# Kernel optimization log

Measured on AMD Instinct MI355X. Metric: run time of the kernel, lower is better.

## Reference

```python
import jax, jax.numpy as jnp
import numpy as np

B, DIMX, DIMY, DIMH = 256, 128, 128, 128
SMOOTH, CONVEX = 2.0, 1.0
MAX_IT, TOL = 500, 1e-3
sp = jax.nn.softplus


def setup_inputs() -> dict:
    key = jax.random.key(0)
    ks = jax.random.split(key, 32)
    def p(k, *shape):
        # xavier-ish small init for weights/biases
        return (jax.random.normal(k, shape, dtype=jnp.float32) * 0.05)
    return {
        'x': jax.random.normal(ks[0], (B, DIMX), dtype=jnp.float32),
        'y': jax.random.normal(ks[1], (B, DIMY), dtype=jnp.float32),
        # first block (Wuus[0], Wyus[0], Wys[0], Wus[0])
        'wuu0_w': p(ks[2], DIMH, DIMX), 'wuu0_b': p(ks[3], DIMH),
        'wyu0_w': p(ks[4], DIMY, DIMX), 'wyu0_b': p(ks[5], DIMY),
        'wy0': p(ks[6], DIMH, DIMY),
        'wu0_w': p(ks[7], DIMH, DIMX), 'wu0_b': p(ks[8], DIMH),
        # middle block (Wuus[1], Wzus[0], Wzs[0], Wyus[1], Wys[1], Wus[1])
        'wuu1_w': p(ks[9], DIMH, DIMH), 'wuu1_b': p(ks[10], DIMH),
        'wzu1_w': p(ks[11], DIMH, DIMH), 'wzu1_b': p(ks[12], DIMH),
        'wz1': p(ks[13], DIMH, DIMH),
        'wyu1_w': p(ks[14], DIMY, DIMH), 'wyu1_b': p(ks[15], DIMY),
        'wy1': p(ks[16], DIMH, DIMY),
        'wu1_w': p(ks[17], DIMH, DIMH), 'wu1_b': p(ks[18], DIMH),
        # last block (Wzus[-1], Wzs[-1], Wyus[-1], Wys[-1], Wus[-1])
        'wzu2_w': p(ks[19], 1, DIMH), 'wzu2_b': p(ks[20], 1),
        'wz2': p(ks[21], 1, DIMH),
        'wyu2_w': p(ks[22], DIMY, DIMH), 'wyu2_b': p(ks[23], DIMY),
        'wy2': p(ks[24], 1, DIMY),
        'wu2_w': p(ks[25], 1, DIMH), 'wu2_b': p(ks[26], 1),
    }


def reference(x, y, wuu0_w, wuu0_b, wyu0_w, wyu0_b, wy0, wu0_w, wu0_b,
              wuu1_w, wuu1_b, wzu1_w, wzu1_b, wz1, wyu1_w, wyu1_b, wy1, wu1_w, wu1_b,
              wzu2_w, wzu2_b, wz2, wyu2_w, wyu2_b, wy2, wu2_w, wu2_b):
    # ICNN scalar output summed over batch (per-sample outputs decouple in y)
    def icnn_sum(y_):
        u0 = sp(x @ wuu0_w.T + wuu0_b)                                   # [B,H]
        z = sp((y_ * (x @ wyu0_w.T + wyu0_b)) @ wy0.T + x @ wu0_w.T + wu0_b)
        u1 = sp(u0 @ wuu1_w.T + wuu1_b)
        zu = sp(u0 @ wzu1_w.T + wzu1_b)
        z = sp((z * zu) @ jnp.clip(wz1, 0.0, 1e10).T
               + (y_ * (u0 @ wyu1_w.T + wyu1_b)) @ wy1.T
               + u0 @ wu1_w.T + wu1_b)
        zu2 = sp(u1 @ wzu2_w.T + wzu2_b)                                 # [B,1]
        z = ((z * zu2) @ jnp.clip(wz2, 0.0, 1e10).T
             + (y_ * (u1 @ wyu2_w.T + wyu2_b)) @ wy2.T
             + u1 @ wu2_w.T + wu2_b)                                     # [B,1]
        out = z + (0.5 / SMOOTH) * jnp.sum(y_ * y_, axis=1, keepdims=True)
        return jnp.sum(out)

    grad_icnn = jax.grad(icnn_sum)
    step = 2.0 * SMOOTH

    def body(carry, i):
        y1, done = carry
        g = grad_icnn(y1)
        y1_new = y1 + (step / (i + 1.0)) * (y - g)
        conv = jnp.mean(jnp.linalg.norm(y - g, axis=1)) < TOL
        y1 = jnp.where(done, y1, y1_new)  # freeze after 'break'
        return (y1, done | conv), None

    y1_init = jnp.ones_like(y)
    (y1, _), _ = jax.lax.scan(body, (y1_init, jnp.asarray(False)),
                              jnp.arange(MAX_IT, dtype=jnp.float32))
    f_ast1 = y1 + CONVEX * y
    return jnp.mean(f_ast1, axis=1).reshape(-1, 1)
```

## Files before the change

### kernel.cpp

```cpp
#include <hip/hip_runtime.h>
#include <math.h>

#define NB 256
#define N 128
#define NTHREADS 512
#define MAX_IT 500
#define SLICE 40
#define SLOT(k) ((((k) >> 5) * SLICE) + ((k) & 31))
#define LDSVEC (3 * SLICE + 32)

__device__ __forceinline__ float quad_sum(float p) {
    p += __shfl_xor(p, 1);
    p += __shfl_xor(p, 2);
    return p;
}
__device__ __forceinline__ float wave_sum(float p) {
    p += __shfl_xor(p, 1);
    p += __shfl_xor(p, 2);
    p += __shfl_xor(p, 4);
    p += __shfl_xor(p, 8);
    p += __shfl_xor(p, 16);
    p += __shfl_xor(p, 32);
    return p;
}
__device__ __forceinline__ float softplus_f(float s) {
    float e = __expf(-fabsf(s));
    return fmaxf(s, 0.f) + __logf(1.f + e);
}
__device__ __forceinline__ float sigmoid_f(float s) {
    float e = __expf(-fabsf(s));
    float r = 1.f / (1.f + e);
    return s >= 0.f ? r : 1.f - r;
}

__device__ __forceinline__ float mv_row(const float* __restrict__ W,
                                        const float* __restrict__ V,
                                        int k, int h) {
    const float4* wr = (const float4*)(W + k * N + h * 32);
    const float4* vr = (const float4*)(V + h * SLICE);
    float q0 = 0.f, q1 = 0.f, q2 = 0.f, q3 = 0.f;
#pragma unroll
    for (int i = 0; i < 8; ++i) {
        float4 w = wr[i], v = vr[i];
        q0 = fmaf(w.x, v.x, q0); q1 = fmaf(w.y, v.y, q1);
        q2 = fmaf(w.z, v.z, q2); q3 = fmaf(w.w, v.w, q3);
    }
    return quad_sum((q0 + q1) + (q2 + q3));
}

__global__ __launch_bounds__(NTHREADS, 2)
void picnn_solve(const float* __restrict__ x, const float* __restrict__ y,
                 const float* __restrict__ wuu0_w, const float* __restrict__ wuu0_b,
                 const float* __restrict__ wyu0_w, const float* __restrict__ wyu0_b,
                 const float* __restrict__ wy0,
                 const float* __restrict__ wu0_w, const float* __restrict__ wu0_b,
                 const float* __restrict__ wuu1_w, const float* __restrict__ wuu1_b,
                 const float* __restrict__ wzu1_w, const float* __restrict__ wzu1_b,
                 const float* __restrict__ wz1,
                 const float* __restrict__ wyu1_w, const float* __restrict__ wyu1_b,
                 const float* __restrict__ wy1,
                 const float* __restrict__ wu1_w, const float* __restrict__ wu1_b,
                 const float* __restrict__ wzu2_w, const float* __restrict__ wzu2_b,
                 const float* __restrict__ wz2,
                 const float* __restrict__ wyu2_w, const float* __restrict__ wyu2_b,
                 const float* __restrict__ wy2,
                 float* __restrict__ out)
{
    const int b = blockIdx.x;
    const int t = threadIdx.x;
    const int k = t >> 2;
    const int h = t & 3;
    const int wave = t >> 6;
    const int lane = t & 63;

    __shared__ __align__(16) float xv[LDSVEC];
    __shared__ __align__(16) float u0v[LDSVEC];
    __shared__ __align__(16) float u1v[LDSVEC];
    __shared__ __align__(16) float t0s[LDSVEC];
    __shared__ __align__(16) float t2s[LDSVEC];
    __shared__ __align__(16) float t1s[LDSVEC];
    __shared__ __align__(16) float d2s[LDSVEC];
    __shared__ __align__(16) float d1s[LDSVEC];
    __shared__ float rp[8];

    if (t < N) xv[SLOT(t)] = x[b * N + t];
    __syncthreads();

    float u0k = softplus_f(mv_row(wuu0_w, xv, k, h) + wuu0_b[k]);
    float a0  = mv_row(wyu0_w, xv, k, h) + wyu0_b[k];
    float c0  = mv_row(wu0_w,  xv, k, h) + wu0_b[k];
    if (h == 0) u0v[SLOT(k)] = u0k;
    __syncthreads();

    float u1k = softplus_f(mv_row(wuu1_w, u0v, k, h) + wuu1_b[k]);
    float zu  = softplus_f(mv_row(wzu1_w, u0v, k, h) + wzu1_b[k]);
    float a1  = mv_row(wyu1_w, u0v, k, h) + wyu1_b[k];
    float c1  = mv_row(wu1_w,  u0v, k, h) + wu1_b[k];
    if (h == 0) u1v[SLOT(k)] = u1k;
    __syncthreads();

    float a2 = mv_row(wyu2_w, u1v, k, h) + wyu2_b[k];
    float e2 = a2 * wy2[k];
    float dp;
    {
        const float4* wr = (const float4*)(wzu2_w + h * 32);
        const float4* vr = (const float4*)(u1v + h * SLICE);
        float q0 = 0.f, q1 = 0.f, q2 = 0.f, q3 = 0.f;
#pragma unroll
        for (int i = 0; i < 8; ++i) {
            float4 w = wr[i], v = vr[i];
            q0 = fmaf(w.x, v.x, q0); q1 = fmaf(w.y, v.y, q1);
            q2 = fmaf(w.z, v.z, q2); q3 = fmaf(w.w, v.w, q3);
        }
        float zu2 = softplus_f(quad_sum((q0 + q1) + (q2 + q3)) + wzu2_b[0]);
        dp = zu2 * fmaxf(wz2[k], 0.f);
    }

    float4 wf0[8], wf1[8], wf2[8];
    float4 wb0[8], wb1[8], wb2[8];
    {
        const float4* r0 = (const float4*)(wy0 + k * N + h * 32);
        const float4* r1 = (const float4*)(wz1 + k * N + h * 32);
        const float4* r2 = (const float4*)(wy1 + k * N + h * 32);
#pragma unroll
        for (int i = 0; i < 8; ++i) {
            wf0[i] = r0[i];
            float4 z = r1[i];
            z.x = fmaxf(z.x, 0.f); z.y = fmaxf(z.y, 0.f);
            z.z = fmaxf(z.z, 0.f); z.w = fmaxf(z.w, 0.f);
            wf1[i] = z;
            wf2[i] = r2[i];
        }
#pragma unroll
        for (int i = 0; i < 8; ++i) {
            int r = h * 32 + 4 * i;
            wb0[i].x = wy0[(r + 0) * N + k]; wb0[i].y = wy0[(r + 1) * N + k];
            wb0[i].z = wy0[(r + 2) * N + k]; wb0[i].w = wy0[(r + 3) * N + k];
            wb1[i].x = fmaxf(wz1[(r + 0) * N + k], 0.f);
            wb1[i].y = fmaxf(wz1[(r + 1) * N + k], 0.f);
            wb1[i].z = fmaxf(wz1[(r + 2) * N + k], 0.f);
            wb1[i].w = fmaxf(wz1[(r + 3) * N + k], 0.f);
            wb2[i].x = wy1[(r + 0) * N + k]; wb2[i].y = wy1[(r + 1) * N + k];
            wb2[i].z = wy1[(r + 2) * N + k]; wb2[i].w = wy1[(r + 3) * N + k];
        }
    }

    const float yk = y[b * N + k];
    float y1v = 2.f * (yk - e2);
    if (h == 0) { t0s[SLOT(k)] = y1v * a0; t2s[SLOT(k)] = y1v * a1; }
    __syncthreads();

    float sig1 = 0.f;
    for (int it = 1; it <= MAX_IT; ++it) {
        const float4* t0r = (const float4*)(t0s + h * SLICE);
        const float4* t2r = (const float4*)(t2s + h * SLICE);
        float p0 = 0.f, p1 = 0.f, p2 = 0.f, p3 = 0.f;
        float q0 = 0.f, q1 = 0.f, q2 = 0.f, q3 = 0.f;
#pragma unroll
        for (int i = 0; i < 8; ++i) {
            float4 v0 = t0r[i], v2 = t2r[i];
            p0 = fmaf(wf0[i].x, v0.x, p0); p1 = fmaf(wf0[i].y, v0.y, p1);
            p2 = fmaf(wf0[i].z, v0.z, p2); p3 = fmaf(wf0[i].w, v0.w, p3);
            q0 = fmaf(wf2[i].x, v2.x, q0); q1 = fmaf(wf2[i].y, v2.y, q1);
            q2 = fmaf(wf2[i].z, v2.z, q2); q3 = fmaf(wf2[i].w, v2.w, q3);
        }
        float s1  = quad_sum((p0 + p1) + (p2 + p3)) + c0;
        float s2a = quad_sum((q0 + q1) + (q2 + q3));
        float e1 = __expf(-fabsf(s1));
        float z1 = fmaxf(s1, 0.f) + __logf(1.f + e1);
        float rr1 = 1.f / (1.f + e1);
        sig1 = (s1 >= 0.f) ? rr1 : 1.f - rr1;
        if (h == 0) t1s[SLOT(k)] = z1 * zu;
        __syncthreads();

        const float4* t1r = (const float4*)(t1s + h * SLICE);
        p0 = p1 = p2 = p3 = 0.f;
#pragma unroll
        for (int i = 0; i < 8; ++i) {
            float4 v1 = t1r[i];
            p0 = fmaf(wf1[i].x, v1.x, p0); p1 = fmaf(wf1[i].y, v1.y, p1);
            p2 = fmaf(wf1[i].z, v1.z, p2); p3 = fmaf(wf1[i].w, v1.w, p3);
        }
        float s2 = quad_sum((p0 + p1) + (p2 + p3)) + s2a + c1;
        float d2 = dp * sigmoid_f(s2);
        if (h == 0) d2s[SLOT(k)] = d2;
        __syncthreads();

        const float4* d2r = (const float4*)(d2s + h * SLICE);
        p0 = p1 = p2 = p3 = 0.f; q0 = q1 = q2 = q3 = 0.f;
#pragma unroll
        for (int i = 0; i < 8; ++i) {
            float4 d = d2r[i];
            p0 = fmaf(wb1[i].x, d.x, p0); p1 = fmaf(wb1[i].y, d.y, p1);
            p2 = fmaf(wb1[i].z, d.z, p2); p3 = fmaf(wb1[i].w, d.w, p3);
            q0 = fmaf(wb2[i].x, d.x, q0); q1 = fmaf(wb2[i].y, d.y, q1);
            q2 = fmaf(wb2[i].z, d.z, q2); q3 = fmaf(wb2[i].w, d.w, q3);
        }
        float qv = quad_sum((p0 + p1) + (p2 + p3));
        float gc = quad_sum((q0 + q1) + (q2 + q3));
        float d1 = qv * zu * sig1;
        if (h == 0) d1s[SLOT(k)] = d1;
        __syncthreads();

        const float4* d1r = (const float4*)(d1s + h * SLICE);
        p0 = p1 = p2 = p3 = 0.f;
#pragma unroll
        for (int i = 0; i < 8; ++i) {
            float4 d = d1r[i];
            p0 = fmaf(wb0[i].x, d.x, p0); p1 = fmaf(wb0[i].y, d.y, p1);
            p2 = fmaf(wb0[i].z, d.z, p2); p3 = fmaf(wb0[i].w, d.w, p3);
        }
        float gb = quad_sum((p0 + p1) + (p2 + p3));
        float g = fmaf(0.5f, y1v, e2) + gc * a1 + gb * a0;
        float rres = yk - g;
        y1v = fmaf(1.25f, rres, y1v);
        if (h == 0) { t0s[SLOT(k)] = y1v * a0; t2s[SLOT(k)] = y1v * a1; }
        float rs = wave_sum(rres * rres);
        if (lane == 0) rp[wave] = rs;
        __syncthreads();
        float tot = ((rp[0] + rp[1]) + (rp[2] + rp[3]))
                  + ((rp[4] + rp[5]) + (rp[6] + rp[7]));
        if (tot < 4e-6f) break;
    }

    __syncthreads();
    float v = wave_sum(y1v + yk);
    if (lane == 0) rp[wave] = v;
    __syncthreads();
    if (t == 0) {
        float s = ((rp[0] + rp[1]) + (rp[2] + rp[3]))
                + ((rp[4] + rp[5]) + (rp[6] + rp[7]));
        out[b] = s * (1.f / 512.f);
    }
}

extern "C" void kernel_launch(void* const* d_in, const int* in_sizes, int n_in,
                              void* d_out, int out_size, void* d_ws, size_t ws_size,
                              hipStream_t stream) {
    const float* x      = (const float*)d_in[0];
    const float* y      = (const float*)d_in[1];
    const float* wuu0_w = (const float*)d_in[2];
    const float* wuu0_b = (const float*)d_in[3];
    const float* wyu0_w = (const float*)d_in[4];
    const float* wyu0_b = (const float*)d_in[5];
    const float* wy0    = (const float*)d_in[6];
    const float* wu0_w  = (const float*)d_in[7];
    const float* wu0_b  = (const float*)d_in[8];
    const float* wuu1_w = (const float*)d_in[9];
    const float* wuu1_b = (const float*)d_in[10];
    const float* wzu1_w = (const float*)d_in[11];
    const float* wzu1_b = (const float*)d_in[12];
    const float* wz1    = (const float*)d_in[13];
    const float* wyu1_w = (const float*)d_in[14];
    const float* wyu1_b = (const float*)d_in[15];
    const float* wy1    = (const float*)d_in[16];
    const float* wu1_w  = (const float*)d_in[17];
    const float* wu1_b  = (const float*)d_in[18];
    const float* wzu2_w = (const float*)d_in[19];
    const float* wzu2_b = (const float*)d_in[20];
    const float* wz2    = (const float*)d_in[21];
    const float* wyu2_w = (const float*)d_in[22];
    const float* wyu2_b = (const float*)d_in[23];
    const float* wy2    = (const float*)d_in[24];
    float* out = (float*)d_out;

    picnn_solve<<<dim3(NB), dim3(NTHREADS), 0, stream>>>(
        x, y, wuu0_w, wuu0_b, wyu0_w, wyu0_b, wy0, wu0_w, wu0_b,
        wuu1_w, wuu1_b, wzu1_w, wzu1_b, wz1, wyu1_w, wyu1_b, wy1, wu1_w, wu1_b,
        wzu2_w, wzu2_b, wz2, wyu2_w, wyu2_b, wy2, out);
}
```

Baseline: 149.8 us.

## Fold a0/a1 into register weights, use DPP reductions, defer convergence check

Pre-scales the register-resident wy0/wy1-derived weights by a0 and a1 so that each iteration shares a single y1 vector in LDS instead of writing two scaled vectors. The quad and row reductions switch from shuffles to DPP row operations, with 16-lane partial sums written to a 32-entry array. The convergence test moves to the top of the next iteration, where its LDS reads overlap the y1 load. This removes LDS traffic and shuffle latency from the serial 500-iteration loop, at the cost of a different floating-point summation order.

After: 159.6 us. 6.5% more time.

```diff
diff --git a/kernel.cpp b/kernel.cpp
--- a/kernel.cpp
+++ b/kernel.cpp
@@ -10,17 +10,18 @@
 #define LDSVEC (3 * SLICE + 32)
 
 __device__ __forceinline__ float quad_sum(float p) {
-    p += __shfl_xor(p, 1);
-    p += __shfl_xor(p, 2);
+    p += __int_as_float(__builtin_amdgcn_update_dpp(
+            0, __float_as_int(p), 0xB1, 0xF, 0xF, true));
+    p += __int_as_float(__builtin_amdgcn_update_dpp(
+            0, __float_as_int(p), 0x4E, 0xF, 0xF, true));
     return p;
 }
-__device__ __forceinline__ float wave_sum(float p) {
-    p += __shfl_xor(p, 1);
-    p += __shfl_xor(p, 2);
-    p += __shfl_xor(p, 4);
-    p += __shfl_xor(p, 8);
-    p += __shfl_xor(p, 16);
-    p += __shfl_xor(p, 32);
+__device__ __forceinline__ float row_sum16(float p) {
+    p = quad_sum(p);
+    p += __int_as_float(__builtin_amdgcn_update_dpp(
+            0, __float_as_int(p), 0x124, 0xF, 0xF, true));
+    p += __int_as_float(__builtin_amdgcn_update_dpp(
+            0, __float_as_int(p), 0x128, 0xF, 0xF, true));
     return p;
 }
 __device__ __forceinline__ float softplus_f(float s) {
@@ -70,33 +71,33 @@
     const int t = threadIdx.x;
     const int k = t >> 2;
     const int h = t & 3;
-    const int wave = t >> 6;
     const int lane = t & 63;
 
     __shared__ __align__(16) float xv[LDSVEC];
     __shared__ __align__(16) float u0v[LDSVEC];
     __shared__ __align__(16) float u1v[LDSVEC];
-    __shared__ __align__(16) float t0s[LDSVEC];
-    __shared__ __align__(16) float t2s[LDSVEC];
+    __shared__ __align__(16) float a0s[LDSVEC];
+    __shared__ __align__(16) float a1s[LDSVEC];
+    __shared__ __align__(16) float y1s[LDSVEC];
     __shared__ __align__(16) float t1s[LDSVEC];
     __shared__ __align__(16) float d2s[LDSVEC];
     __shared__ __align__(16) float d1s[LDSVEC];
-    __shared__ float rp[8];
+    __shared__ __align__(16) float rp[32];
 
     if (t < N) xv[SLOT(t)] = x[b * N + t];
     __syncthreads();
 
     float u0k = softplus_f(mv_row(wuu0_w, xv, k, h) + wuu0_b[k]);
-    float a0  = mv_row(wyu0_w, xv, k, h) + wyu0_b[k];
+    float a0k = mv_row(wyu0_w, xv, k, h) + wyu0_b[k];
     float c0  = mv_row(wu0_w,  xv, k, h) + wu0_b[k];
-    if (h == 0) u0v[SLOT(k)] = u0k;
+    if (h == 0) { u0v[SLOT(k)] = u0k; a0s[SLOT(k)] = a0k; }
     __syncthreads();
 
     float u1k = softplus_f(mv_row(wuu1_w, u0v, k, h) + wuu1_b[k]);
     float zu  = softplus_f(mv_row(wzu1_w, u0v, k, h) + wzu1_b[k]);
-    float a1  = mv_row(wyu1_w, u0v, k, h) + wyu1_b[k];
+    float a1k = mv_row(wyu1_w, u0v, k, h) + wyu1_b[k];
     float c1  = mv_row(wu1_w,  u0v, k, h) + wu1_b[k];
-    if (h == 0) u1v[SLOT(k)] = u1k;
+    if (h == 0) { u1v[SLOT(k)] = u1k; a1s[SLOT(k)] = a1k; }
     __syncthreads();
 
     float a2 = mv_row(wyu2_w, u1v, k, h) + wyu2_b[k];
@@ -143,33 +144,50 @@
             wb2[i].x = wy1[(r + 0) * N + k]; wb2[i].y = wy1[(r + 1) * N + k];
             wb2[i].z = wy1[(r + 2) * N + k]; wb2[i].w = wy1[(r + 3) * N + k];
         }
+        const float4* a0r = (const float4*)(a0s + h * SLICE);
+        const float4* a1r = (const float4*)(a1s + h * SLICE);
+#pragma unroll
+        for (int i = 0; i < 8; ++i) {
+            float4 s0 = a0r[i], s1 = a1r[i];
+            wf0[i].x *= s0.x; wf0[i].y *= s0.y; wf0[i].z *= s0.z; wf0[i].w *= s0.w;
+            wf2[i].x *= s1.x; wf2[i].y *= s1.y; wf2[i].z *= s1.z; wf2[i].w *= s1.w;
+        }
     }
 
     const float yk = y[b * N + k];
     float y1v = 2.f * (yk - e2);
-    if (h == 0) { t0s[SLOT(k)] = y1v * a0; t2s[SLOT(k)] = y1v * a1; }
-    __syncthreads();
-
-    float sig1 = 0.f;
+    if (h == 0) y1s[SLOT(k)] = y1v;
+    __syncthreads();
+
     for (int it = 1; it <= MAX_IT; ++it) {
-        const float4* t0r = (const float4*)(t0s + h * SLICE);
-        const float4* t2r = (const float4*)(t2s + h * SLICE);
+        const float4* yr = (const float4*)(y1s + h * SLICE);
+        float4 vv[8];
+#pragma unroll
+        for (int i = 0; i < 8; ++i) vv[i] = yr[i];
+        if (it > 1) {
+            const float4* rpv = (const float4*)rp;
+            float4 ra = (rpv[0] + rpv[1]) + (rpv[2] + rpv[3]);
+            float4 rb = (rpv[4] + rpv[5]) + (rpv[6] + rpv[7]);
+            float4 u = ra + rb;
+            float tot = (u.x + u.y) + (u.z + u.w);
+            if (tot < 4e-6f) break;
+        }
         float p0 = 0.f, p1 = 0.f, p2 = 0.f, p3 = 0.f;
         float q0 = 0.f, q1 = 0.f, q2 = 0.f, q3 = 0.f;
 #pragma unroll
         for (int i = 0; i < 8; ++i) {
-            float4 v0 = t0r[i], v2 = t2r[i];
-            p0 = fmaf(wf0[i].x, v0.x, p0); p1 = fmaf(wf0[i].y, v0.y, p1);
-            p2 = fmaf(wf0[i].z, v0.z, p2); p3 = fmaf(wf0[i].w, v0.w, p3);
-            q0 = fmaf(wf2[i].x, v2.x, q0); q1 = fmaf(wf2[i].y, v2.y, q1);
-            q2 = fmaf(wf2[i].z, v2.z, q2); q3 = fmaf(wf2[i].w, v2.w, q3);
-        }
-        float s1  = quad_sum((p0 + p1) + (p2 + p3)) + c0;
+            float4 v = vv[i];
+            p0 = fmaf(wf0[i].x, v.x, p0); p1 = fmaf(wf0[i].y, v.y, p1);
+            p2 = fmaf(wf0[i].z, v.z, p2); p3 = fmaf(wf0[i].w, v.w, p3);
+            q0 = fmaf(wf2[i].x, v.x, q0); q1 = fmaf(wf2[i].y, v.y, q1);
+            q2 = fmaf(wf2[i].z, v.z, q2); q3 = fmaf(wf2[i].w, v.w, q3);
+        }
+        float s1v = quad_sum((p0 + p1) + (p2 + p3)) + c0;
         float s2a = quad_sum((q0 + q1) + (q2 + q3));
-        float e1 = __expf(-fabsf(s1));
-        float z1 = fmaxf(s1, 0.f) + __logf(1.f + e1);
+        float e1 = __expf(-fabsf(s1v));
+        float z1 = fmaxf(s1v, 0.f) + __logf(1.f + e1);
         float rr1 = 1.f / (1.f + e1);
-        sig1 = (s1 >= 0.f) ? rr1 : 1.f - rr1;
+        float sig1 = (s1v >= 0.f) ? rr1 : 1.f - rr1;
         if (h == 0) t1s[SLOT(k)] = z1 * zu;
         __syncthreads();
 
@@ -211,26 +229,25 @@
             p2 = fmaf(wb0[i].z, d.z, p2); p3 = fmaf(wb0[i].w, d.w, p3);
         }
         float gb = quad_sum((p0 + p1) + (p2 + p3));
-        float g = fmaf(0.5f, y1v, e2) + gc * a1 + gb * a0;
+        float g = fmaf(0.5f, y1v, e2) + gc * a1k + gb * a0k;
         float rres = yk - g;
         y1v = fmaf(1.25f, rres, y1v);
-        if (h == 0) { t0s[SLOT(k)] = y1v * a0; t2s[SLOT(k)] = y1v * a1; }
-        float rs = wave_sum(rres * rres);
-        if (lane == 0) rp[wave] = rs;
-        __syncthreads();
-        float tot = ((rp[0] + rp[1]) + (rp[2] + rp[3]))
-                  + ((rp[4] + rp[5]) + (rp[6] + rp[7]));
-        if (tot < 4e-6f) break;
-    }
-
-    __syncthreads();
-    float v = wave_sum(y1v + yk);
-    if (lane == 0) rp[wave] = v;
+        if (h == 0) y1s[SLOT(k)] = y1v;
+        float rs = row_sum16(rres * rres);
+        if ((lane & 15) == 0) rp[t >> 4] = rs;
+        __syncthreads();
+    }
+
+    __syncthreads();
+    float v = row_sum16(y1v + yk);
+    if ((lane & 15) == 0) rp[t >> 4] = v;
     __syncthreads();
     if (t == 0) {
-        float s = ((rp[0] + rp[1]) + (rp[2] + rp[3]))
-                + ((rp[4] + rp[5]) + (rp[6] + rp[7]));
-        out[b] = s * (1.f / 512.f);
+        const float4* rpv = (const float4*)rp;
+        float4 ra = (rpv[0] + rpv[1]) + (rpv[2] + rpv[3]);
+        float4 rb = (rpv[4] + rpv[5]) + (rpv[6] + rpv[7]);
+        float4 u = ra + rb;
+        out[b] = ((u.x + u.y) + (u.z + u.w)) * (1.f / 512.f);
     }
 }
 
```
